# Kernel tuning notes

Measured on AMD Instinct MI355X. Metric: run time of the kernel, lower is better.

Reference implementation:

```python
import jax, jax.numpy as jnp
import numpy as np

N = 12000
E = 384000
F_IN, F_HID, F_OUT = 4, 50, 1433
NEG_SLOPE = 0.2  # PyG GATConv default leaky_relu slope


def gat_conv(x, W, a_src, a_dst, b, src, dst):
    """PyG GATConv (heads=1, concat=True) with self-loops already appended.
    x: [N, Fin], W: [Fin, Fout], a_src/a_dst/b: [Fout], src/dst: [E']."""
    h = x @ W                                   # [N, Fout]
    al = h @ a_src                              # [N] per-source logit part
    ar = h @ a_dst                              # [N] per-target logit part
    e = jax.nn.leaky_relu(al[src] + ar[dst], NEG_SLOPE)   # [E'] edge logits
    # segment softmax over edges grouped by destination node
    m = jax.ops.segment_max(e, dst, num_segments=N)       # [N]
    ex = jnp.exp(e - m[dst])
    s = jax.ops.segment_sum(ex, dst, num_segments=N)      # [N]
    alpha = ex / s[dst]                         # [E'] (self-loops => s > 0)
    out = jax.ops.segment_sum(alpha[:, None] * h[src], dst, num_segments=N)
    return out + b


def setup_inputs() -> dict:
    key = jax.random.key(0)
    ks = jax.random.split(key, 10)
    x = jax.random.normal(ks[0], (N, F_IN), dtype=jnp.float32)
    edge_index = jax.random.randint(ks[1], (2, E), 0, N, dtype=jnp.int32)
    # Glorot-ish init for params
    W1 = jax.random.normal(ks[2], (F_IN, F_HID), dtype=jnp.float32) / np.sqrt(F_IN)
    a_src1 = jax.random.normal(ks[3], (F_HID,), dtype=jnp.float32) / np.sqrt(F_HID)
    a_dst1 = jax.random.normal(ks[4], (F_HID,), dtype=jnp.float32) / np.sqrt(F_HID)
    b1 = jnp.zeros((F_HID,), dtype=jnp.float32)
    W2 = jax.random.normal(ks[5], (F_HID, F_OUT), dtype=jnp.float32) / np.sqrt(F_HID)
    a_src2 = jax.random.normal(ks[6], (F_OUT,), dtype=jnp.float32) / np.sqrt(F_OUT)
    a_dst2 = jax.random.normal(ks[7], (F_OUT,), dtype=jnp.float32) / np.sqrt(F_OUT)
    b2 = jnp.zeros((F_OUT,), dtype=jnp.float32)
    return {"x": x, "edge_index": edge_index, "W1": W1, "a_src1": a_src1,
            "a_dst1": a_dst1, "b1": b1, "W2": W2, "a_src2": a_src2,
            "a_dst2": a_dst2, "b2": b2}


def reference(x, edge_index, W1, a_src1, a_dst1, b1, W2, a_src2, a_dst2, b2):
    # PyG GATConv adds self-loops by default
    loops = jnp.arange(N, dtype=edge_index.dtype)
    src = jnp.concatenate([edge_index[0], loops])
    dst = jnp.concatenate([edge_index[1], loops])
    h = jax.nn.relu(gat_conv(x, W1, a_src1, a_dst1, b1, src, dst))
    h = jax.nn.relu(gat_conv(h, W2, a_src2, a_dst2, b2, src, dst))
    adj_pred = jax.nn.sigmoid(h @ h.T)          # InnerProductDecoder.forward_all
    return (adj_pred, edge_index)
```

## Files before the change

### kernel.cpp

```cpp
#include <hip/hip_runtime.h>
#include <hip/hip_bf16.h>

#define NNODES 12000
#define NEDGES 384000
#define NETOT  (NEDGES + NNODES)
#define FIN    4
#define FHID   50
#define FOUT   1433
#define KP     1440
#define MP     12032
#define NEG_SLOPE 0.2f

typedef __hip_bfloat16 bf16_t;
typedef float f32x4 __attribute__((ext_vector_type(4)));
typedef float f32x2 __attribute__((ext_vector_type(2)));

__device__ __forceinline__ float  b2f(bf16_t h) { return __bfloat162float(h); }
__device__ __forceinline__ bf16_t f2b(float f)  { return __float2bfloat16(f); }

__global__ void k_init(int* __restrict__ deg, unsigned char* __restrict__ h2) {
    int i = blockIdx.x * blockDim.x + threadIdx.x;
    int stride = gridDim.x * blockDim.x;
    for (int v = i; v < NNODES; v += stride) deg[v] = 1;
    const size_t padN = (size_t)(MP - NNODES) * KP;
    for (size_t t = i; t < padN; t += stride) h2[(size_t)NNODES * KP + t] = 0;
}

__global__ void k_count(const int* __restrict__ ei, int* __restrict__ deg) {
    int i = blockIdx.x * blockDim.x + threadIdx.x;
    if (i < NEDGES) atomicAdd(&deg[ei[NEDGES + i]], 1);
}

__global__ __launch_bounds__(1024) void k_scan(const int* __restrict__ deg, int* __restrict__ rowptr) {
    __shared__ int sd[1024];
    __shared__ int carry;
    int tid = threadIdx.x;
    if (tid == 0) { carry = 0; rowptr[0] = 0; }
    __syncthreads();
    for (int base = 0; base < NNODES; base += 1024) {
        int v = (base + tid < NNODES) ? deg[base + tid] : 0;
        sd[tid] = v;
        __syncthreads();
        for (int off = 1; off < 1024; off <<= 1) {
            int t = (tid >= off) ? sd[tid - off] : 0;
            __syncthreads();
            sd[tid] += t;
            __syncthreads();
        }
        int inc = sd[tid] + carry;
        if (base + tid < NNODES) rowptr[base + tid + 1] = inc;
        __syncthreads();
        if (tid == 1023) carry = sd[1023] + carry;
        __syncthreads();
    }
}

__global__ void k_cursor(const int* __restrict__ rowptr, int* __restrict__ cursor) {
    int i = blockIdx.x * blockDim.x + threadIdx.x;
    if (i < NNODES) cursor[i] = rowptr[i];
}

__global__ void k_fill(const int* __restrict__ ei, int* __restrict__ cursor, int* __restrict__ csrc) {
    int i = blockIdx.x * blockDim.x + threadIdx.x;
    if (i < NETOT) {
        int s, d;
        if (i < NEDGES) { s = ei[i]; d = ei[NEDGES + i]; }
        else            { s = d = i - NEDGES; }
        int pos = atomicAdd(&cursor[d], 1);
        csrc[pos] = s;
    }
}

__global__ __launch_bounds__(256) void k_linear1(
        const bf16_t* __restrict__ x, const bf16_t* __restrict__ W1,
        const bf16_t* __restrict__ as1, const bf16_t* __restrict__ ad1,
        float* __restrict__ h1pre, float* __restrict__ al, float* __restrict__ ar) {
    __shared__ float sW[FIN * FHID];
    __shared__ float sa[FHID], sdl[FHID];
    int tid = threadIdx.x;
    if (tid < FIN * FHID) sW[tid] = b2f(W1[tid]);
    if (tid < FHID) { sa[tid] = b2f(as1[tid]); sdl[tid] = b2f(ad1[tid]); }
    __syncthreads();
    int i = blockIdx.x * 256 + tid;
    if (i >= NNODES) return;
    float x0 = b2f(x[i * 4 + 0]), x1 = b2f(x[i * 4 + 1]);
    float x2 = b2f(x[i * 4 + 2]), x3 = b2f(x[i * 4 + 3]);
    float hal = 0.f, har = 0.f;
    for (int j = 0; j < FHID; ++j) {
        float h = x0 * sW[j] + x1 * sW[FHID + j] + x2 * sW[2 * FHID + j] + x3 * sW[3 * FHID + j];
        h1pre[(size_t)i * FHID + j] = h;
        hal += h * sa[j];
        har += h * sdl[j];
    }
    al[i] = hal; ar[i] = har;
}

__global__ __launch_bounds__(64) void k_agg1(
        const float* __restrict__ h1pre, const float* __restrict__ al, const float* __restrict__ ar,
        const int* __restrict__ rowptr, const int* __restrict__ csrc,
        const bf16_t* __restrict__ b1, float* __restrict__ h1) {
    int v = blockIdx.x, tid = threadIdx.x;
    int s0 = rowptr[v], s1 = rowptr[v + 1];
    float arv = ar[v];
    float m = -1e30f;
    for (int e = s0 + tid; e < s1; e += 64) {
        float l = al[csrc[e]] + arv;
        l = l > 0.f ? l : NEG_SLOPE * l;
        m = fmaxf(m, l);
    }
#pragma unroll
    for (int off = 32; off; off >>= 1) m = fmaxf(m, __shfl_xor(m, off, 64));
    __shared__ float sw[64];
    __shared__ int ssrc[64];
    float acc = 0.f, ssum = 0.f;
    for (int base = s0; base < s1; base += 64) {
        int e = base + tid;
        float w = 0.f; int si = 0;
        if (e < s1) {
            si = csrc[e];
            float l = al[si] + arv;
            l = l > 0.f ? l : NEG_SLOPE * l;
            w = __expf(l - m);
        }
        ssum += w;
        sw[tid] = w; ssrc[tid] = si;
        __syncthreads();
        int cnt = min(64, s1 - base);
        if (tid < FHID) {
#pragma unroll 4
            for (int j = 0; j < cnt; ++j)
                acc += sw[j] * h1pre[(size_t)ssrc[j] * FHID + tid];
        }
        __syncthreads();
    }
#pragma unroll
    for (int off = 32; off; off >>= 1) ssum += __shfl_xor(ssum, off, 64);
    if (tid < FHID) {
        float o = acc / ssum + b2f(b1[tid]);
        h1[(size_t)v * FHID + tid] = fmaxf(o, 0.f);
    }
}

__global__ __launch_bounds__(256) void k_linear2(
        const float* __restrict__ h1, const bf16_t* __restrict__ W2,
        const bf16_t* __restrict__ as2, const bf16_t* __restrict__ ad2,
        unsigned char* __restrict__ h2pre, float* __restrict__ al2, float* __restrict__ ar2) {
    int v0 = blockIdx.x * 4, tid = threadIdx.x;
    __shared__ float sh[4][FHID];
    if (tid < 4 * FHID) sh[tid / FHID][tid % FHID] = h1[(size_t)v0 * FHID + tid];
    __syncthreads();
    float pal[4] = {0.f, 0.f, 0.f, 0.f}, par[4] = {0.f, 0.f, 0.f, 0.f};
#pragma unroll
    for (int i = 0; i < 3; ++i) {
        int f0 = i * 512 + 2 * tid;
        if (f0 < KP) {
            float d0[4] = {0.f, 0.f, 0.f, 0.f}, d1[4] = {0.f, 0.f, 0.f, 0.f};
            bool ok0 = f0 < FOUT, ok1 = f0 + 1 < FOUT;
            if (ok0) {
                int f1 = ok1 ? f0 + 1 : f0;
#pragma unroll 10
                for (int k = 0; k < FHID; ++k) {
                    float w0 = b2f(W2[k * FOUT + f0]);
                    float w1 = b2f(W2[k * FOUT + f1]);
#pragma unroll
                    for (int c = 0; c < 4; ++c) {
                        d0[c] += sh[c][k] * w0;
                        d1[c] += sh[c][k] * w1;
                    }
                }
                if (!ok1) { d1[0] = d1[1] = d1[2] = d1[3] = 0.f; }
                float sa0 = b2f(as2[f0]), sd0 = b2f(ad2[f0]);
                float sa1 = ok1 ? b2f(as2[f0 + 1]) : 0.f;
                float sd1 = ok1 ? b2f(ad2[f0 + 1]) : 0.f;
#pragma unroll
                for (int c = 0; c < 4; ++c) {
                    pal[c] += d0[c] * sa0 + d1[c] * sa1;
                    par[c] += d0[c] * sd0 + d1[c] * sd1;
                }
            }
#pragma unroll
            for (int c = 0; c < 4; ++c) {
                int pk = __builtin_amdgcn_cvt_pk_fp8_f32(d0[c], d1[c], 0, false);
                *(unsigned short*)(h2pre + (size_t)(v0 + c) * KP + f0) = (unsigned short)pk;
            }
        }
    }
#pragma unroll
    for (int off = 32; off; off >>= 1)
#pragma unroll
        for (int c = 0; c < 4; ++c) {
            pal[c] += __shfl_xor(pal[c], off, 64);
            par[c] += __shfl_xor(par[c], off, 64);
        }
    __shared__ float rA[4][4], rB[4][4];
    int wave = tid >> 6, lane = tid & 63;
    if (lane == 0)
#pragma unroll
        for (int c = 0; c < 4; ++c) { rA[wave][c] = pal[c]; rB[wave][c] = par[c]; }
    __syncthreads();
    if (tid < 4) {
        al2[v0 + tid] = rA[0][tid] + rA[1][tid] + rA[2][tid] + rA[3][tid];
        ar2[v0 + tid] = rB[0][tid] + rB[1][tid] + rB[2][tid] + rB[3][tid];
    }
}

__global__ __launch_bounds__(256) void k_agg2(
        const unsigned char* __restrict__ h2pre, const float* __restrict__ al, const float* __restrict__ ar,
        const int* __restrict__ rowptr, const int* __restrict__ csrc,
        const bf16_t* __restrict__ bias2, unsigned char* __restrict__ h2) {
    int v = blockIdx.x, tid = threadIdx.x;
    int s0 = rowptr[v], s1 = rowptr[v + 1];
    float arv = ar[v];
    float m = -1e30f;
    for (int e = s0 + tid; e < s1; e += 256) {
        float l = al[csrc[e]] + arv;
        l = l > 0.f ? l : NEG_SLOPE * l;
        m = fmaxf(m, l);
    }
#pragma unroll
    for (int off = 32; off; off >>= 1) m = fmaxf(m, __shfl_xor(m, off, 64));
    __shared__ float red[4];
    int wave = tid >> 6, lane = tid & 63;
    if (lane == 0) red[wave] = m;
    __syncthreads();
    m = fmaxf(fmaxf(red[0], red[1]), fmaxf(red[2], red[3]));
    __syncthreads();

    float acc[8] = {0.f, 0.f, 0.f, 0.f, 0.f, 0.f, 0.f, 0.f};
    float ssum = 0.f;
    __shared__ float sw[256];
    __shared__ int ssrc[256];
    const bool act = tid < (KP / 8);
    for (int base = s0; base < s1; base += 256) {
        int e = base + tid;
        float w = 0.f; int si = 0;
        if (e < s1) {
            si = csrc[e];
            float l = al[si] + arv;
            l = l > 0.f ? l : NEG_SLOPE * l;
            w = __expf(l - m);
        }
        ssum += w;
        sw[tid] = w; ssrc[tid] = si;
        __syncthreads();
        int cnt = min(256, s1 - base);
        if (act) {
#pragma unroll 4
            for (int j = 0; j < cnt; ++j) {
                float wj = sw[j];
                const uint2* hp = (const uint2*)(h2pre + (size_t)ssrc[j] * KP);
                uint2 p = hp[tid];
                f32x2 e0 = __builtin_amdgcn_cvt_pk_f32_fp8(p.x, false);
                f32x2 e1 = __builtin_amdgcn_cvt_pk_f32_fp8(p.x, true);
                f32x2 e2 = __builtin_amdgcn_cvt_pk_f32_fp8(p.y, false);
                f32x2 e3 = __builtin_amdgcn_cvt_pk_f32_fp8(p.y, true);
                acc[0] += wj * e0.x; acc[1] += wj * e0.y;
                acc[2] += wj * e1.x; acc[3] += wj * e1.y;
                acc[4] += wj * e2.x; acc[5] += wj * e2.y;
                acc[6] += wj * e3.x; acc[7] += wj * e3.y;
            }
        }
        __syncthreads();
    }
#pragma unroll
    for (int off = 32; off; off >>= 1) ssum += __shfl_xor(ssum, off, 64);
    if (lane == 0) red[wave] = ssum;
    __syncthreads();
    float inv = 1.f / (red[0] + red[1] + red[2] + red[3]);

    if (act) {
        int fb = 8 * tid;
        float o[8];
#pragma unroll
        for (int t = 0; t < 8; ++t) {
            int f = fb + t;
            o[t] = (f < FOUT) ? fmaxf(acc[t] * inv + b2f(bias2[f]), 0.f) : 0.f;
        }
        uint2 pk;
        int w0 = __builtin_amdgcn_cvt_pk_fp8_f32(o[0], o[1], 0, false);
        pk.x = (unsigned)__builtin_amdgcn_cvt_pk_fp8_f32(o[2], o[3], w0, true);
        int w1 = __builtin_amdgcn_cvt_pk_fp8_f32(o[4], o[5], 0, false);
        pk.y = (unsigned)__builtin_amdgcn_cvt_pk_fp8_f32(o[6], o[7], w1, true);
        *(uint2*)(h2 + (size_t)v * KP + fb) = pk;
    }
}

__global__ __launch_bounds__(256) void k_gemm_sig(const unsigned char* __restrict__ Hm,
                                                  float* __restrict__ out) {
    const int bx = blockIdx.x, by = blockIdx.y;
    if (bx < by) return;
    __shared__ __align__(16) unsigned char As[128 * 32];
    __shared__ __align__(16) unsigned char Bs[128 * 32];
    const int tid = threadIdx.x;
    const int wave = tid >> 6;
    const int lane = tid & 63;
    const int rowA0 = by * 128;
    const int rowB0 = bx * 128;

    const int sRow = wave * 32 + (lane >> 1);
    const int sOff = (lane & 1) * 16;
    const unsigned char* gA = Hm + (size_t)(rowA0 + sRow) * KP + sOff;
    const unsigned char* gB = Hm + (size_t)(rowB0 + sRow) * KP + sOff;
    const int ldsOff = wave * 1024 + lane * 16;

    f32x4 acc[4][4] = {};

    const int wrow = wave >> 1, wcol = wave & 1;
    const int r = lane & 15, q = lane >> 4;

    for (int kt = 0; kt < KP / 32; ++kt) {
        const int k0 = kt * 32;
        __builtin_amdgcn_global_load_lds(
            (const __attribute__((address_space(1))) void*)(gA + k0),
            (__attribute__((address_space(3))) void*)(As + ldsOff), 16, 0, 0);
        __builtin_amdgcn_global_load_lds(
            (const __attribute__((address_space(1))) void*)(gB + k0),
            (__attribute__((address_space(3))) void*)(Bs + ldsOff), 16, 0, 0);
        __syncthreads();
        long af[4], bfr[4];
#pragma unroll
        for (int mi = 0; mi < 4; ++mi)
            af[mi] = *(const long*)(As + (wrow * 64 + mi * 16 + r) * 32 + q * 8);
#pragma unroll
        for (int ni = 0; ni < 4; ++ni)
            bfr[ni] = *(const long*)(Bs + (wcol * 64 + ni * 16 + r) * 32 + q * 8);
#pragma unroll
        for (int mi = 0; mi < 4; ++mi)
#pragma unroll
            for (int ni = 0; ni < 4; ++ni)
                acc[mi][ni] = __builtin_amdgcn_mfma_f32_16x16x32_fp8_fp8(af[mi], bfr[ni], acc[mi][ni], 0, 0, 0);
        __syncthreads();
    }

#pragma unroll
    for (int mi = 0; mi < 4; ++mi) {
        const int row0 = rowA0 + wrow * 64 + mi * 16 + q * 4;
#pragma unroll
        for (int ni = 0; ni < 4; ++ni) {
            const int col = rowB0 + wcol * 64 + ni * 16 + r;
            if (col < NNODES && row0 < NNODES) {
                f32x4 s;
#pragma unroll
                for (int r2 = 0; r2 < 4; ++r2)
                    s[r2] = 1.f / (1.f + __expf(-acc[mi][ni][r2]));
#pragma unroll
                for (int r2 = 0; r2 < 4; ++r2)
                    out[(size_t)(row0 + r2) * NNODES + col] = s[r2];
                if (bx != by)
                    *(f32x4*)(out + (size_t)col * NNODES + row0) = s;
            }
        }
    }
}

__global__ void k_edges(const int* __restrict__ ei, float* __restrict__ outbase) {
    int i = blockIdx.x * blockDim.x + threadIdx.x;
    if (i < 2 * NEDGES)
        outbase[(size_t)NNODES * (size_t)NNODES + (size_t)i] = (float)ei[i];
}

extern "C" void kernel_launch(void* const* d_in, const int* in_sizes, int n_in,
                              void* d_out, int out_size, void* d_ws, size_t ws_size,
                              hipStream_t stream) {
    const bf16_t* x   = (const bf16_t*)d_in[0];
    const int*    ei  = (const int*)d_in[1];
    const bf16_t* W1  = (const bf16_t*)d_in[2];
    const bf16_t* as1 = (const bf16_t*)d_in[3];
    const bf16_t* ad1 = (const bf16_t*)d_in[4];
    const bf16_t* b1  = (const bf16_t*)d_in[5];
    const bf16_t* W2  = (const bf16_t*)d_in[6];
    const bf16_t* as2 = (const bf16_t*)d_in[7];
    const bf16_t* ad2 = (const bf16_t*)d_in[8];
    const bf16_t* b2  = (const bf16_t*)d_in[9];
    float* out = (float*)d_out;

    char* obuf = (char*)d_out;
    size_t off = 0;
    auto carve = [&](size_t bytes) {
        char* p = obuf + off;
        off += (bytes + 255) & ~(size_t)255;
        return p;
    };
    float* h1pre  = (float*)carve((size_t)NNODES * FHID * 4);
    float* al1    = (float*)carve((size_t)NNODES * 4);
    float* ar1    = (float*)carve((size_t)NNODES * 4);
    float* h1     = (float*)carve((size_t)NNODES * FHID * 4);
    float* al2    = (float*)carve((size_t)NNODES * 4);
    float* ar2    = (float*)carve((size_t)NNODES * 4);
    int*   deg    = (int*)carve((size_t)NNODES * 4);
    int*   rowptr = (int*)carve((size_t)(NNODES + 1) * 4);
    int*   cursor = (int*)carve((size_t)NNODES * 4);
    int*   csrc   = (int*)carve((size_t)NETOT * 4);
    unsigned char* h2pre = (unsigned char*)carve((size_t)NNODES * KP);
    unsigned char* h2 = (unsigned char*)d_ws;
    (void)ws_size; (void)in_sizes; (void)n_in; (void)out_size;

    hipLaunchKernelGGL(k_init,    dim3(256), dim3(256), 0, stream, deg, h2);
    hipLaunchKernelGGL(k_count,   dim3((NEDGES + 255) / 256), dim3(256), 0, stream, ei, deg);
    hipLaunchKernelGGL(k_scan,    dim3(1), dim3(1024), 0, stream, deg, rowptr);
    hipLaunchKernelGGL(k_cursor,  dim3((NNODES + 255) / 256), dim3(256), 0, stream, rowptr, cursor);
    hipLaunchKernelGGL(k_fill,    dim3((NETOT + 255) / 256), dim3(256), 0, stream, ei, cursor, csrc);
    hipLaunchKernelGGL(k_linear1, dim3((NNODES + 255) / 256), dim3(256), 0, stream,
                       x, W1, as1, ad1, h1pre, al1, ar1);
    hipLaunchKernelGGL(k_agg1,    dim3(NNODES), dim3(64), 0, stream,
                       h1pre, al1, ar1, rowptr, csrc, b1, h1);
    hipLaunchKernelGGL(k_linear2, dim3(NNODES / 4), dim3(256), 0, stream,
                       h1, W2, as2, ad2, h2pre, al2, ar2);
    hipLaunchKernelGGL(k_agg2,    dim3(NNODES), dim3(256), 0, stream,
                       h2pre, al2, ar2, rowptr, csrc, b2, h2);
    hipLaunchKernelGGL(k_gemm_sig, dim3(MP / 128, MP / 128), dim3(256), 0, stream, h2, out);
    hipLaunchKernelGGL(k_edges,   dim3((2 * NEDGES + 255) / 256), dim3(256), 0, stream, ei, out);
}
```

Before: 1.257 ms.

## Switch decoder GEMM to bf16 MFMA with swizzled LDS and triangular grid

The second-layer output h2 is now stored in bf16 instead of fp8. The h·hᵀ decoder GEMM uses bf16 16x16x32 MFMA with an XOR-swizzled LDS layout to avoid bank conflicts. The 2D grid, where half the blocks exited early, becomes a 1D launch over upper-triangular tiles. The agg2 inner loop unroll also goes from 4 to 8. This trades twice the GEMM operand bytes and half the MFMA throughput of fp8 for better precision, plus less block-scheduling waste and fewer LDS conflicts.

New measurement: 1.173 ms. 6.7% less time.

```diff
diff --git a/kernel.cpp b/kernel.cpp
--- a/kernel.cpp
+++ b/kernel.cpp
@@ -9,21 +9,25 @@
 #define FOUT   1433
 #define KP     1440
 #define MP     12032
+#define NTILE  (MP / 128)
+#define NTRI   (NTILE * (NTILE + 1) / 2)
 #define NEG_SLOPE 0.2f
 
 typedef __hip_bfloat16 bf16_t;
+typedef __bf16 bf16x8 __attribute__((ext_vector_type(8)));
 typedef float f32x4 __attribute__((ext_vector_type(4)));
 typedef float f32x2 __attribute__((ext_vector_type(2)));
 
 __device__ __forceinline__ float  b2f(bf16_t h) { return __bfloat162float(h); }
 __device__ __forceinline__ bf16_t f2b(float f)  { return __float2bfloat16(f); }
-
-__global__ void k_init(int* __restrict__ deg, unsigned char* __restrict__ h2) {
+__device__ __forceinline__ unsigned short f2bu(float f) { bf16_t h = f2b(f); return *(unsigned short*)&h; }
+
+__global__ void k_init(int* __restrict__ deg, bf16_t* __restrict__ h2) {
     int i = blockIdx.x * blockDim.x + threadIdx.x;
     int stride = gridDim.x * blockDim.x;
     for (int v = i; v < NNODES; v += stride) deg[v] = 1;
     const size_t padN = (size_t)(MP - NNODES) * KP;
-    for (size_t t = i; t < padN; t += stride) h2[(size_t)NNODES * KP + t] = 0;
+    for (size_t t = i; t < padN; t += stride) h2[(size_t)NNODES * KP + t] = f2b(0.f);
 }
 
 __global__ void k_count(const int* __restrict__ ei, int* __restrict__ deg) {
@@ -207,7 +211,7 @@
 __global__ __launch_bounds__(256) void k_agg2(
         const unsigned char* __restrict__ h2pre, const float* __restrict__ al, const float* __restrict__ ar,
         const int* __restrict__ rowptr, const int* __restrict__ csrc,
-        const bf16_t* __restrict__ bias2, unsigned char* __restrict__ h2) {
+        const bf16_t* __restrict__ bias2, bf16_t* __restrict__ h2) {
     int v = blockIdx.x, tid = threadIdx.x;
     int s0 = rowptr[v], s1 = rowptr[v + 1];
     float arv = ar[v];
@@ -245,7 +249,7 @@
         __syncthreads();
         int cnt = min(256, s1 - base);
         if (act) {
-#pragma unroll 4
+#pragma unroll 8
             for (int j = 0; j < cnt; ++j) {
                 float wj = sw[j];
                 const uint2* hp = (const uint2*)(h2pre + (size_t)ssrc[j] * KP);
@@ -270,65 +274,78 @@
 
     if (act) {
         int fb = 8 * tid;
-        float o[8];
+        unsigned short o[8];
 #pragma unroll
         for (int t = 0; t < 8; ++t) {
             int f = fb + t;
-            o[t] = (f < FOUT) ? fmaxf(acc[t] * inv + b2f(bias2[f]), 0.f) : 0.f;
-        }
-        uint2 pk;
-        int w0 = __builtin_amdgcn_cvt_pk_fp8_f32(o[0], o[1], 0, false);
-        pk.x = (unsigned)__builtin_amdgcn_cvt_pk_fp8_f32(o[2], o[3], w0, true);
-        int w1 = __builtin_amdgcn_cvt_pk_fp8_f32(o[4], o[5], 0, false);
-        pk.y = (unsigned)__builtin_amdgcn_cvt_pk_fp8_f32(o[6], o[7], w1, true);
-        *(uint2*)(h2 + (size_t)v * KP + fb) = pk;
-    }
-}
-
-__global__ __launch_bounds__(256) void k_gemm_sig(const unsigned char* __restrict__ Hm,
+            o[t] = f2bu((f < FOUT) ? fmaxf(acc[t] * inv + b2f(bias2[f]), 0.f) : 0.f);
+        }
+        uint4 pk;
+        pk.x = (unsigned)o[0] | ((unsigned)o[1] << 16);
+        pk.y = (unsigned)o[2] | ((unsigned)o[3] << 16);
+        pk.z = (unsigned)o[4] | ((unsigned)o[5] << 16);
+        pk.w = (unsigned)o[6] | ((unsigned)o[7] << 16);
+        *(uint4*)(h2 + (size_t)v * KP + fb) = pk;
+    }
+}
+
+__global__ __launch_bounds__(256) void k_gemm_sig(const bf16_t* __restrict__ Hm,
                                                   float* __restrict__ out) {
-    const int bx = blockIdx.x, by = blockIdx.y;
-    if (bx < by) return;
-    __shared__ __align__(16) unsigned char As[128 * 32];
-    __shared__ __align__(16) unsigned char Bs[128 * 32];
+    int t = blockIdx.x;
+    int by = (int)((2 * NTILE + 1 - sqrtf((float)(2 * NTILE + 1) * (2 * NTILE + 1) - 8.0f * t)) * 0.5f);
+    if (by < 0) by = 0;
+    if (by > NTILE - 1) by = NTILE - 1;
+    while (by + 1 < NTILE && (by + 1) * NTILE - ((by + 1) * by) / 2 <= t) ++by;
+    while (by > 0 && by * NTILE - (by * (by - 1)) / 2 > t) --by;
+    int bx = by + (t - (by * NTILE - (by * (by - 1)) / 2));
+
+    __shared__ __align__(16) bf16_t As[128 * 32];
+    __shared__ __align__(16) bf16_t Bs[128 * 32];
     const int tid = threadIdx.x;
     const int wave = tid >> 6;
     const int lane = tid & 63;
     const int rowA0 = by * 128;
     const int rowB0 = bx * 128;
 
-    const int sRow = wave * 32 + (lane >> 1);
-    const int sOff = (lane & 1) * 16;
-    const unsigned char* gA = Hm + (size_t)(rowA0 + sRow) * KP + sOff;
-    const unsigned char* gB = Hm + (size_t)(rowB0 + sRow) * KP + sOff;
-    const int ldsOff = wave * 1024 + lane * 16;
+    const int sRow  = wave * 16 + (lane >> 2);
+    const int sSlot = (lane & 3) ^ ((lane >> 2) & 3);
+    const bf16_t* gA = Hm + (size_t)(rowA0 + sRow) * KP + sSlot * 8;
+    const bf16_t* gB = Hm + (size_t)(rowB0 + sRow) * KP + sSlot * 8;
 
     f32x4 acc[4][4] = {};
 
     const int wrow = wave >> 1, wcol = wave & 1;
     const int r = lane & 15, q = lane >> 4;
+    const int rslot = q ^ (r & 3);
+    const __bf16* Asb = (const __bf16*)As;
+    const __bf16* Bsb = (const __bf16*)Bs;
 
     for (int kt = 0; kt < KP / 32; ++kt) {
         const int k0 = kt * 32;
-        __builtin_amdgcn_global_load_lds(
-            (const __attribute__((address_space(1))) void*)(gA + k0),
-            (__attribute__((address_space(3))) void*)(As + ldsOff), 16, 0, 0);
-        __builtin_amdgcn_global_load_lds(
-            (const __attribute__((address_space(1))) void*)(gB + k0),
-            (__attribute__((address_space(3))) void*)(Bs + ldsOff), 16, 0, 0);
-        __syncthreads();
-        long af[4], bfr[4];
+#pragma unroll
+        for (int c = 0; c < 2; ++c) {
+            __builtin_amdgcn_global_load_lds(
+                (const __attribute__((address_space(1))) void*)(gA + (size_t)c * 64 * KP + k0),
+                (__attribute__((address_space(3))) void*)((char*)As + c * 4096 + wave * 1024),
+                16, 0, 0);
+            __builtin_amdgcn_global_load_lds(
+                (const __attribute__((address_space(1))) void*)(gB + (size_t)c * 64 * KP + k0),
+                (__attribute__((address_space(3))) void*)((char*)Bs + c * 4096 + wave * 1024),
+                16, 0, 0);
+        }
+        __syncthreads();
+        bf16x8 af[4], bfr[4];
 #pragma unroll
         for (int mi = 0; mi < 4; ++mi)
-            af[mi] = *(const long*)(As + (wrow * 64 + mi * 16 + r) * 32 + q * 8);
+            af[mi] = *(const bf16x8*)(Asb + ((wrow * 64 + mi * 16 + r) * 32 + rslot * 8));
 #pragma unroll
         for (int ni = 0; ni < 4; ++ni)
-            bfr[ni] = *(const long*)(Bs + (wcol * 64 + ni * 16 + r) * 32 + q * 8);
+            bfr[ni] = *(const bf16x8*)(Bsb + ((wcol * 64 + ni * 16 + r) * 32 + rslot * 8));
 #pragma unroll
         for (int mi = 0; mi < 4; ++mi)
 #pragma unroll
             for (int ni = 0; ni < 4; ++ni)
-                acc[mi][ni] = __builtin_amdgcn_mfma_f32_16x16x32_fp8_fp8(af[mi], bfr[ni], acc[mi][ni], 0, 0, 0);
+                acc[mi][ni] = __builtin_amdgcn_mfma_f32_16x16x32_bf16(af[mi], bfr[ni], acc[mi][ni], 0, 0, 0);
         __syncthreads();
     }
 
@@ -392,7 +409,7 @@
     int*   cursor = (int*)carve((size_t)NNODES * 4);
     int*   csrc   = (int*)carve((size_t)NETOT * 4);
     unsigned char* h2pre = (unsigned char*)carve((size_t)NNODES * KP);
-    unsigned char* h2 = (unsigned char*)d_ws;
+    bf16_t* h2 = (bf16_t*)d_ws;
     (void)ws_size; (void)in_sizes; (void)n_in; (void)out_size;
 
     hipLaunchKernelGGL(k_init,    dim3(256), dim3(256), 0, stream, deg, h2);
@@ -408,6 +425,6 @@
                        h1, W2, as2, ad2, h2pre, al2, ar2);
     hipLaunchKernelGGL(k_agg2,    dim3(NNODES), dim3(256), 0, stream,
                        h2pre, al2, ar2, rowptr, csrc, b2, h2);
-    hipLaunchKernelGGL(k_gemm_sig, dim3(MP / 128, MP / 128), dim3(256), 0, stream, h2, out);
+    hipLaunchKernelGGL(k_gemm_sig, dim3(NTRI), dim3(256), 0, stream, h2, out);
     hipLaunchKernelGGL(k_edges,   dim3((2 * NEDGES + 255) / 256), dim3(256), 0, stream, ei, out);
 }
```
